# Optimization experiments

Hardware: AMD Instinct MI355X
Metric: run time of the kernel (lower is better)

The kernel has to match this reference:

```python
import jax, jax.numpy as jnp
import numpy as np

B = 16384      # batch size
D = 512        # state_dim (= number of graph nodes)
HID = 512      # hidden_dim of main GCN blocks
EH = 32        # hidden dim of ENSO GCN blocks
K = 2          # fourier_modes
OMEGA = 2.0 * np.pi / 12.0


def setup_inputs() -> dict:
    ks = jax.random.split(jax.random.key(0), 20)
    def w(k, shape, scale=0.05):
        return (jax.random.normal(k, shape) * scale).astype(jnp.float32)
    inp = {
        "x": jax.random.normal(ks[0], (B, D), dtype=jnp.float32),
        "t": jax.random.uniform(ks[1], (1,), dtype=jnp.float32) * 12.0,
        "fourier_coeffs": w(ks[2], (D, D, 2 * K + 1), 0.1),
        # quadratic_graph: GCN(D->HID) -> ReLU -> GCN(HID->D)
        "quad_W1": w(ks[3], (D, HID)), "quad_b1": jnp.zeros((HID,), jnp.float32),
        "quad_W2": w(ks[4], (HID, D)), "quad_b2": jnp.zeros((D,), jnp.float32),
        # cubic_graph
        "cubic_W1": w(ks[5], (D, HID)), "cubic_b1": jnp.zeros((HID,), jnp.float32),
        "cubic_W2": w(ks[6], (HID, D)), "cubic_b2": jnp.zeros((D,), jnp.float32),
        # enso_T_graph: GCN(5->32) -> ReLU -> GCN(32->1)
        "ensoT_W1": w(ks[7], (5, EH)), "ensoT_b1": jnp.zeros((EH,), jnp.float32),
        "ensoT_W2": w(ks[8], (EH, 1)), "ensoT_b2": jnp.zeros((1,), jnp.float32),
        # enso_H_graph
        "ensoH_W1": w(ks[9], (5, EH)), "ensoH_b1": jnp.zeros((EH,), jnp.float32),
        "ensoH_W2": w(ks[10], (EH, 1)), "ensoH_b2": jnp.zeros((1,), jnp.float32),
    }
    return inp


def _gcn2(feat, W1, b1, W2, b2):
    # Fully-connected graph + self-loops => normalized adjacency P = (1/N) 11^T.
    # All node rows are identical (x expanded over nodes), so P @ X == X and every
    # node's output is identical: the 2-layer GCN collapses to two dense GEMMs.
    h = jax.nn.relu(feat @ W1 + b1)
    return h @ W2 + b2


def reference(x, t, fourier_coeffs,
              quad_W1, quad_b1, quad_W2, quad_b2,
              cubic_W1, cubic_b1, cubic_W2, cubic_b2,
              ensoT_W1, ensoT_b1, ensoT_W2, ensoT_b2,
              ensoH_W1, ensoH_b1, ensoH_W2, ensoH_b2):
    ts = t[0]
    # --- Seasonal linear operator L(t) = C0 + sum_k Ck^c cos(k w t) + Ck^s sin(k w t)
    L = fourier_coeffs[:, :, 0]
    for k in range(1, K + 1):
        L = L + fourier_coeffs[:, :, 2 * k - 1] * jnp.cos(k * OMEGA * ts)
        L = L + fourier_coeffs[:, :, 2 * k] * jnp.sin(k * OMEGA * ts)
    linear_term = jnp.einsum('ij,bj->bi', L, x)  # [B, D]

    # --- Graph nonlinear terms (per-node outputs identical; mean over feature dim)
    quad = _gcn2(x, quad_W1, quad_b1, quad_W2, quad_b2)        # [B, D]
    cubic = _gcn2(x, cubic_W1, cubic_b1, cubic_W2, cubic_b2)   # [B, D]
    # torch: out[node] identical for all nodes; .mean(dim=1) over features -> same
    # scalar replicated across the state dimension.
    quad_terms = jnp.broadcast_to(quad.mean(axis=1, keepdims=True), (x.shape[0], D))
    cubic_terms = jnp.broadcast_to(cubic.mean(axis=1, keepdims=True), (x.shape[0], D))
    nonlinear = quad_terms + cubic_terms

    # --- ENSO-specific physics (state_dim >= 2)
    T = x[:, 0:1]
    H = x[:, 1:2]
    fT = jnp.concatenate([T, H, T * T, T * H, T * T * T], axis=1)   # [B, 5]
    fH = jnp.concatenate([T, H, T * T, T * H, T * H * H], axis=1)   # [B, 5]
    cT = _gcn2(fT, ensoT_W1, ensoT_b1, ensoT_W2, ensoT_b2)  # [B, 1]
    cH = _gcn2(fH, ensoH_W1, ensoH_b1, ensoH_W2, ensoH_b2)  # [B, 1]
    pad = jnp.zeros((x.shape[0], D - 2), dtype=x.dtype)
    nonlinear = nonlinear + jnp.concatenate([cT, cH, pad], axis=1)

    return linear_term + nonlinear
```

## Files before the change

### kernel.cpp

```cpp
#include <hip/hip_runtime.h>


#define OMEGA_F 0.5235987755982988f

typedef __attribute__((ext_vector_type(8))) short short8;
typedef __attribute__((ext_vector_type(4))) float f32x4;

__device__ __forceinline__ unsigned short f2bf(float f) {
  union { float f; unsigned int u; } a;
  a.f = f;
  unsigned int u = a.u;
  return (unsigned short)((u + 0x7fffu + ((u >> 16) & 1u)) >> 16);
}

__device__ __forceinline__ void gload16(const void* g, void* l) {
  __builtin_amdgcn_global_load_lds(
      (const __attribute__((address_space(1))) unsigned int*)g,
      (__attribute__((address_space(3))) unsigned int*)l, 16, 0, 0);
}

__global__ void prep_conv(const float* __restrict__ fc, const float* __restrict__ qW1,
                          const float* __restrict__ cW1, const float* __restrict__ t,
                          const float* __restrict__ qW2, const float* __restrict__ cW2,
                          const float* __restrict__ qb2, const float* __restrict__ cb2,
                          const float4* __restrict__ x4, const float* __restrict__ x,
                          const float* __restrict__ tW1, const float* __restrict__ tb1,
                          const float* __restrict__ tW2, const float* __restrict__ tb2,
                          const float* __restrict__ hW1, const float* __restrict__ hb1,
                          const float* __restrict__ hW2, const float* __restrict__ hb2,
                          unsigned short* __restrict__ WT, uint2* __restrict__ xb,
                          float* __restrict__ qw2m, float* __restrict__ cw2m,
                          float* __restrict__ b2m, float* __restrict__ cT,
                          float* __restrict__ cH, float* __restrict__ rowadd) {
  int b = blockIdx.x, tdx = threadIdx.x;
  if (b < 3072) {
    int idx = b * 256 + tdx;
    int n = idx >> 9;
    int k = idx & 511;
    float v;
    if (n < 512) {
      float th = OMEGA_F * t[0];
      float s1, c1, s2, c2;
      sincosf(th, &s1, &c1);
      sincosf(2.0f * th, &s2, &c2);
      const float* p = fc + ((size_t)n * 512 + k) * 5;
      v = p[0] + p[1] * c1 + p[2] * s1 + p[3] * c2 + p[4] * s2;
    } else if (n < 1024) {
      v = qW1[(size_t)k * 512 + (n - 512)];
    } else {
      v = cW1[(size_t)k * 512 + (n - 1024)];
    }
    WT[idx] = f2bf(v);
  } else if (b < 3076) {
    int bb = b - 3072;
    const float* W = (bb < 2) ? qW2 : cW2;
    float* o = (bb < 2) ? qw2m : cw2m;
    int h = (bb & 1) * 256 + tdx;
    const float4* row = (const float4*)(W + (size_t)h * 512);
    float s = 0.f;
    for (int i = 0; i < 128; ++i) { float4 v = row[i]; s += (v.x + v.y) + (v.z + v.w); }
    o[h] = s * (1.0f / 512.0f);
  } else if (b == 3076) {
    __shared__ float sm[256];
    sm[tdx] = qb2[tdx] + qb2[tdx + 256];
    __syncthreads();
    for (int w = 128; w > 0; w >>= 1) { if (tdx < w) sm[tdx] += sm[tdx + w]; __syncthreads(); }
    if (tdx == 0) b2m[0] = sm[0] * (1.0f / 512.0f);
    __syncthreads();
    sm[tdx] = cb2[tdx] + cb2[tdx + 256];
    __syncthreads();
    for (int w = 128; w > 0; w >>= 1) { if (tdx < w) sm[tdx] += sm[tdx + w]; __syncthreads(); }
    if (tdx == 0) b2m[1] = sm[0] * (1.0f / 512.0f);
  } else if (b < 3077 + 8192) {
    int i = (b - 3077) * 256 + tdx;
    float4 v = x4[i];
    uint2 r;
    r.x = (unsigned)f2bf(v.x) | ((unsigned)f2bf(v.y) << 16);
    r.y = (unsigned)f2bf(v.z) | ((unsigned)f2bf(v.w) << 16);
    xb[i] = r;
  } else {
    int row = (b - 11269) * 256 + tdx;
    rowadd[row] = 0.f;
    float T = x[(size_t)row * 512];
    float H = x[(size_t)row * 512 + 1];
    float fT[5] = {T, H, T * T, T * H, T * T * T};
    float fH[5] = {T, H, T * T, T * H, T * H * H};
    float sT = tb2[0], sH = hb2[0];
#pragma unroll 4
    for (int e = 0; e < 32; ++e) {
      float a1 = tb1[e], a2 = hb1[e];
#pragma unroll
      for (int f = 0; f < 5; ++f) {
        a1 += fT[f] * tW1[f * 32 + e];
        a2 += fH[f] * hW1[f * 32 + e];
      }
      sT += fmaxf(a1, 0.f) * tW2[e];
      sH += fmaxf(a2, 0.f) * hW2[e];
    }
    cT[row] = sT;
    cH[row] = sH;
  }
}

#define GEMM_MAINLOOP(A_, Bt_, MB_, NB_)                                          \
  const int tid = threadIdx.x;                                                    \
  const int lane = tid & 63;                                                      \
  const int wave = tid >> 6;                                                      \
  const int wm = wave & 1;                                                        \
  const int wn = wave >> 1;                                                       \
  const int m_base = (MB_);                                                       \
  const int n_base = (NB_);                                                       \
  const int lrow = lane & 15;                                                     \
  const int l7 = lrow & 7;                                                        \
  const int kgrp = lane >> 4;                                                     \
  const int srow = lane >> 3;                                                     \
  const int sk = ((lane & 7) ^ srow) * 8;                                         \
  const unsigned short* gA0 = (A_) + (size_t)(m_base + wave * 8 + srow) * 512 + sk; \
  const unsigned short* gA1 = gA0 + 32 * 512;                                     \
  const unsigned short* gA2 = gA0 + 64 * 512;                                     \
  const unsigned short* gA3 = gA0 + 96 * 512;                                     \
  const unsigned short* gB0 = (Bt_) + (size_t)(n_base + wave * 8 + srow) * 512 + sk;\
  const unsigned short* gB1 = gB0 + 32 * 512;                                     \
  const unsigned short* gB2 = gB0 + 64 * 512;                                     \
  const unsigned short* gB3 = gB0 + 96 * 512;                                     \
  unsigned short* lA0 = As + wave * 512;                                          \
  unsigned short* lA1 = As + (4 + wave) * 512;                                    \
  unsigned short* lA2 = As + (8 + wave) * 512;                                    \
  unsigned short* lA3 = As + (12 + wave) * 512;                                   \
  unsigned short* lB0 = Bs + wave * 512;                                          \
  unsigned short* lB1 = Bs + (4 + wave) * 512;                                    \
  unsigned short* lB2 = Bs + (8 + wave) * 512;                                    \
  unsigned short* lB3 = Bs + (12 + wave) * 512;                                   \
  f32x4 acc[4][4];                                                                \
  _Pragma("unroll") for (int i = 0; i < 4; ++i)                                   \
      _Pragma("unroll") for (int j = 0; j < 4; ++j)                               \
          acc[i][j] = (f32x4){0.f, 0.f, 0.f, 0.f};                                \
  for (int k0 = 0; k0 < 512; k0 += 64) {                                          \
    gload16(gA0, lA0); gload16(gA1, lA1); gload16(gA2, lA2); gload16(gA3, lA3);   \
    gload16(gB0, lB0); gload16(gB1, lB1); gload16(gB2, lB2); gload16(gB3, lB3);   \
    gA0 += 64; gA1 += 64; gA2 += 64; gA3 += 64;                                   \
    gB0 += 64; gB1 += 64; gB2 += 64; gB3 += 64;                                   \
    __syncthreads();                                                              \
    _Pragma("unroll") for (int h = 0; h < 2; ++h) {                               \
      short8 af[4], bfr[4];                                                       \
      const int ks = ((h * 4 + kgrp) ^ l7) * 8;                                   \
      _Pragma("unroll") for (int i = 0; i < 4; ++i)                               \
          af[i] = *(const short8*)(&As[(wm * 64 + i * 16 + lrow) * 64 + ks]);     \
      _Pragma("unroll") for (int j = 0; j < 4; ++j)                               \
          bfr[j] = *(const short8*)(&Bs[(wn * 64 + j * 16 + lrow) * 64 + ks]);    \
      _Pragma("unroll") for (int i = 0; i < 4; ++i)                               \
          _Pragma("unroll") for (int j = 0; j < 4; ++j)                           \
              acc[i][j] = __builtin_amdgcn_mfma_f32_16x16x32_bf16(af[i], bfr[j],  \
                                                                  acc[i][j], 0, 0, 0); \
    }                                                                             \
    __syncthreads();                                                              \
  }

__global__ __launch_bounds__(256) void nl_gemm(
    const unsigned short* __restrict__ A,
    const unsigned short* __restrict__ Bt,
    const float* __restrict__ qb1, const float* __restrict__ cb1,
    const float* __restrict__ qw2m, const float* __restrict__ cw2m,
    float* __restrict__ rowadd) {
  __shared__ unsigned short As[128 * 64];
  __shared__ unsigned short Bs[128 * 64];
  float rs[4][4];
#pragma unroll
  for (int i = 0; i < 4; ++i)
#pragma unroll
    for (int r = 0; r < 4; ++r) rs[i][r] = 0.f;

  for (int t = 0; t < 2; ++t) {
    GEMM_MAINLOOP(A, Bt, blockIdx.x * 128, (blockIdx.y * 2 + t) * 128)
    const bool isq = (n_base < 512);
    const float* b1 = isq ? qb1 : cb1;
    const float* w2m = isq ? qw2m : cw2m;
    const int cb0 = (isq ? n_base : n_base - 512) + wn * 64 + lrow;
#pragma unroll
    for (int j = 0; j < 4; ++j) {
      int col = cb0 + j * 16;
      float bb = b1[col];
      float ww = w2m[col];
#pragma unroll
      for (int i = 0; i < 4; ++i)
#pragma unroll
        for (int r = 0; r < 4; ++r)
          rs[i][r] += fmaxf(acc[i][j][r] + bb, 0.f) * ww;
    }
  }

  const int lane_e = threadIdx.x & 63;
  const int wm_e = (threadIdx.x >> 6) & 1;
  const int rbase = blockIdx.x * 128 + wm_e * 64 + (lane_e >> 4) * 4;
#pragma unroll
  for (int i = 0; i < 4; ++i)
#pragma unroll
    for (int r = 0; r < 4; ++r) {
      float v = rs[i][r];
      v += __shfl_xor(v, 1, 64);
      v += __shfl_xor(v, 2, 64);
      v += __shfl_xor(v, 4, 64);
      v += __shfl_xor(v, 8, 64);
      if ((lane_e & 15) == 0) atomicAdd(&rowadd[rbase + i * 16 + r], v);
    }
}

__global__ __launch_bounds__(256) void lin_gemm(
    const unsigned short* __restrict__ A,
    const unsigned short* __restrict__ Bt,
    const float* __restrict__ rowadd, const float* __restrict__ b2m,
    const float* __restrict__ cT, const float* __restrict__ cH,
    float* __restrict__ out) {
  __shared__ unsigned short As[128 * 64];
  __shared__ unsigned short Bs[128 * 64];
  GEMM_MAINLOOP(A, Bt, blockIdx.x * 128, blockIdx.y * 128)
  const int rbase = m_base + wm * 64 + (lane >> 4) * 4;
  const float b2s = b2m[0] + b2m[1];
  float ra[4][4];
#pragma unroll
  for (int i = 0; i < 4; ++i)
#pragma unroll
    for (int r = 0; r < 4; ++r) ra[i][r] = rowadd[rbase + i * 16 + r] + b2s;
#pragma unroll
  for (int j = 0; j < 4; ++j) {
    int col = n_base + wn * 64 + j * 16 + lrow;
#pragma unroll
    for (int i = 0; i < 4; ++i)
#pragma unroll
      for (int r = 0; r < 4; ++r) {
        int row = rbase + i * 16 + r;
        float v = acc[i][j][r] + ra[i][r];
        if (col == 0) v += cT[row];
        if (col == 1) v += cH[row];
        out[(size_t)row * 512 + col] = v;
      }
  }
}

extern "C" void kernel_launch(void* const* d_in, const int* in_sizes, int n_in,
                              void* d_out, int out_size, void* d_ws, size_t ws_size,
                              hipStream_t stream) {
  const float* x   = (const float*)d_in[0];
  const float* t   = (const float*)d_in[1];
  const float* fc  = (const float*)d_in[2];
  const float* qW1 = (const float*)d_in[3];
  const float* qb1 = (const float*)d_in[4];
  const float* qW2 = (const float*)d_in[5];
  const float* qb2 = (const float*)d_in[6];
  const float* cW1 = (const float*)d_in[7];
  const float* cb1 = (const float*)d_in[8];
  const float* cW2 = (const float*)d_in[9];
  const float* cb2 = (const float*)d_in[10];
  const float* tW1 = (const float*)d_in[11];
  const float* tb1 = (const float*)d_in[12];
  const float* tW2 = (const float*)d_in[13];
  const float* tb2 = (const float*)d_in[14];
  const float* hW1 = (const float*)d_in[15];
  const float* hb1 = (const float*)d_in[16];
  const float* hW2 = (const float*)d_in[17];
  const float* hb2 = (const float*)d_in[18];
  float* out = (float*)d_out;

  char* ws = (char*)d_ws;
  unsigned short* WT = (unsigned short*)(ws);
  unsigned short* xb = (unsigned short*)(ws + 1572864);
  float* qw2m   = (float*)(ws + 18350080);
  float* cw2m   = (float*)(ws + 18352128);
  float* b2m    = (float*)(ws + 18354176);
  float* cT     = (float*)(ws + 18354432);
  float* cH     = (float*)(ws + 18419968);
  float* rowadd = (float*)(ws + 18485504);

  prep_conv<<<11333, 256, 0, stream>>>(fc, qW1, cW1, t, qW2, cW2, qb2, cb2,
                                       (const float4*)x, x,
                                       tW1, tb1, tW2, tb2, hW1, hb1, hW2, hb2,
                                       WT, (uint2*)xb, qw2m, cw2m, b2m, cT, cH,
                                       rowadd);
  nl_gemm<<<dim3(128, 4), 256, 0, stream>>>(xb, WT + (size_t)512 * 512,
                                            qb1, cb1, qw2m, cw2m, rowadd);
  lin_gemm<<<dim3(128, 4), 256, 0, stream>>>(xb, WT, rowadd, b2m, cT, cH, out);
}
```

Before: 171.7 us.

## Fuse nonlinear and linear GEMMs into one kernel with per-row-block counters

Merges the nonlinear GEMM (which reduces into rowadd via atomics) and the linear GEMM into a single kernel. Each block first does its nonlinear share, bumps a per-row-block counter, then runs its linear tile and spin-waits until all four column blocks of that row block have contributed before reading rowadd. This removes one kernel launch and the global barrier between them, and lets the linear GEMM overlap with other blocks' nonlinear work. It relies on all 512 blocks being co-resident (launch_bounds 2 per CU) to avoid deadlock, and adds spin-wait and fence costs.

```diff
diff --git a/kernel.cpp b/kernel.cpp
--- a/kernel.cpp
+++ b/kernel.cpp
@@ -31,7 +31,8 @@
                           unsigned short* __restrict__ WT, uint2* __restrict__ xb,
                           float* __restrict__ qw2m, float* __restrict__ cw2m,
                           float* __restrict__ b2m, float* __restrict__ cT,
-                          float* __restrict__ cH, float* __restrict__ rowadd) {
+                          float* __restrict__ cH, float* __restrict__ rowadd,
+                          unsigned int* __restrict__ cnt) {
   int b = blockIdx.x, tdx = threadIdx.x;
   if (b < 3072) {
     int idx = b * 256 + tdx;
@@ -62,6 +63,7 @@
     o[h] = s * (1.0f / 512.0f);
   } else if (b == 3076) {
     __shared__ float sm[256];
+    if (tdx < 128) cnt[tdx] = 0;
     sm[tdx] = qb2[tdx] + qb2[tdx + 256];
     __syncthreads();
     for (int w = 128; w > 0; w >>= 1) { if (tdx < w) sm[tdx] += sm[tdx + w]; __syncthreads(); }
@@ -156,14 +158,18 @@
     __syncthreads();                                                              \
   }
 
-__global__ __launch_bounds__(256) void nl_gemm(
+__global__ __launch_bounds__(256, 2) void fused_gemm(
     const unsigned short* __restrict__ A,
-    const unsigned short* __restrict__ Bt,
+    const unsigned short* __restrict__ WT,
     const float* __restrict__ qb1, const float* __restrict__ cb1,
     const float* __restrict__ qw2m, const float* __restrict__ cw2m,
-    float* __restrict__ rowadd) {
+    float* __restrict__ rowadd, const float* __restrict__ b2m,
+    const float* __restrict__ cT, const float* __restrict__ cH,
+    float* __restrict__ out, unsigned int* __restrict__ cnt) {
   __shared__ unsigned short As[128 * 64];
   __shared__ unsigned short Bs[128 * 64];
+  const unsigned short* Bnl = WT + (size_t)512 * 512;
+
   float rs[4][4];
 #pragma unroll
   for (int i = 0; i < 4; ++i)
@@ -171,7 +177,7 @@
     for (int r = 0; r < 4; ++r) rs[i][r] = 0.f;
 
   for (int t = 0; t < 2; ++t) {
-    GEMM_MAINLOOP(A, Bt, blockIdx.x * 128, (blockIdx.y * 2 + t) * 128)
+    GEMM_MAINLOOP(A, Bnl, blockIdx.x * 128, (blockIdx.y * 2 + t) * 128)
     const bool isq = (n_base < 512);
     const float* b1 = isq ? qb1 : cb1;
     const float* w2m = isq ? qw2m : cw2m;
@@ -189,51 +195,62 @@
     }
   }
 
-  const int lane_e = threadIdx.x & 63;
-  const int wm_e = (threadIdx.x >> 6) & 1;
-  const int rbase = blockIdx.x * 128 + wm_e * 64 + (lane_e >> 4) * 4;
-#pragma unroll
-  for (int i = 0; i < 4; ++i)
-#pragma unroll
-    for (int r = 0; r < 4; ++r) {
-      float v = rs[i][r];
-      v += __shfl_xor(v, 1, 64);
-      v += __shfl_xor(v, 2, 64);
-      v += __shfl_xor(v, 4, 64);
-      v += __shfl_xor(v, 8, 64);
-      if ((lane_e & 15) == 0) atomicAdd(&rowadd[rbase + i * 16 + r], v);
-    }
-}
-
-__global__ __launch_bounds__(256) void lin_gemm(
-    const unsigned short* __restrict__ A,
-    const unsigned short* __restrict__ Bt,
-    const float* __restrict__ rowadd, const float* __restrict__ b2m,
-    const float* __restrict__ cT, const float* __restrict__ cH,
-    float* __restrict__ out) {
-  __shared__ unsigned short As[128 * 64];
-  __shared__ unsigned short Bs[128 * 64];
-  GEMM_MAINLOOP(A, Bt, blockIdx.x * 128, blockIdx.y * 128)
-  const int rbase = m_base + wm * 64 + (lane >> 4) * 4;
-  const float b2s = b2m[0] + b2m[1];
-  float ra[4][4];
-#pragma unroll
-  for (int i = 0; i < 4; ++i)
-#pragma unroll
-    for (int r = 0; r < 4; ++r) ra[i][r] = rowadd[rbase + i * 16 + r] + b2s;
-#pragma unroll
-  for (int j = 0; j < 4; ++j) {
-    int col = n_base + wn * 64 + j * 16 + lrow;
+  {
+    const int lane_e = threadIdx.x & 63;
+    const int wm_e = (threadIdx.x >> 6) & 1;
+    const int rbase = blockIdx.x * 128 + wm_e * 64 + (lane_e >> 4) * 4;
 #pragma unroll
     for (int i = 0; i < 4; ++i)
 #pragma unroll
       for (int r = 0; r < 4; ++r) {
-        int row = rbase + i * 16 + r;
-        float v = acc[i][j][r] + ra[i][r];
-        if (col == 0) v += cT[row];
-        if (col == 1) v += cH[row];
-        out[(size_t)row * 512 + col] = v;
+        float v = rs[i][r];
+        v += __shfl_xor(v, 1, 64);
+        v += __shfl_xor(v, 2, 64);
+        v += __shfl_xor(v, 4, 64);
+        v += __shfl_xor(v, 8, 64);
+        if ((lane_e & 15) == 0) atomicAdd(&rowadd[rbase + i * 16 + r], v);
       }
+  }
+  __syncthreads();
+  if (threadIdx.x == 0) {
+    __threadfence();
+    atomicAdd(&cnt[blockIdx.x], 1u);
+  }
+
+  {
+    GEMM_MAINLOOP(A, WT, blockIdx.x * 128, blockIdx.y * 128)
+
+    if (wave == 0) {
+      while (__hip_atomic_load(&cnt[blockIdx.x], __ATOMIC_ACQUIRE,
+                               __HIP_MEMORY_SCOPE_AGENT) < 4u) {
+        __builtin_amdgcn_s_sleep(2);
+      }
+    }
+    __syncthreads();
+
+    const int rbase = m_base + wm * 64 + (lane >> 4) * 4;
+    const float b2s = b2m[0] + b2m[1];
+    float ra[4][4];
+#pragma unroll
+    for (int i = 0; i < 4; ++i)
+#pragma unroll
+      for (int r = 0; r < 4; ++r)
+        ra[i][r] = __hip_atomic_load(&rowadd[rbase + i * 16 + r],
+                                     __ATOMIC_RELAXED, __HIP_MEMORY_SCOPE_AGENT) + b2s;
+#pragma unroll
+    for (int j = 0; j < 4; ++j) {
+      int col = n_base + wn * 64 + j * 16 + lrow;
+#pragma unroll
+      for (int i = 0; i < 4; ++i)
+#pragma unroll
+        for (int r = 0; r < 4; ++r) {
+          int row = rbase + i * 16 + r;
+          float v = acc[i][j][r] + ra[i][r];
+          if (col == 0) v += cT[row];
+          if (col == 1) v += cH[row];
+          out[(size_t)row * 512 + col] = v;
+        }
+    }
   }
 }
 
@@ -270,13 +287,13 @@
   float* cT     = (float*)(ws + 18354432);
   float* cH     = (float*)(ws + 18419968);
   float* rowadd = (float*)(ws + 18485504);
+  unsigned int* cnt = (unsigned int*)(ws + 18551040);
 
   prep_conv<<<11333, 256, 0, stream>>>(fc, qW1, cW1, t, qW2, cW2, qb2, cb2,
                                        (const float4*)x, x,
                                        tW1, tb1, tW2, tb2, hW1, hb1, hW2, hb2,
                                        WT, (uint2*)xb, qw2m, cw2m, b2m, cT, cH,
-                                       rowadd);
-  nl_gemm<<<dim3(128, 4), 256, 0, stream>>>(xb, WT + (size_t)512 * 512,
-                                            qb1, cb1, qw2m, cw2m, rowadd);
-  lin_gemm<<<dim3(128, 4), 256, 0, stream>>>(xb, WT, rowadd, b2m, cT, cH, out);
-}
+                                       rowadd, cnt);
+  fused_gemm<<<dim3(128, 4), 256, 0, stream>>>(xb, WT, qb1, cb1, qw2m, cw2m,
+                                               rowadd, b2m, cT, cH, out, cnt);
+}
```

Measured after the change: 182.6 us. 1.06x slower.

## Widen nl_gemm tile to 128x256 so each A tile is loaded once

Applied to the files above, without the earlier changes.

The nonlinear GEMM kernel no longer runs two sequential 128x128 passes over the same A rows. It now loads one A tile and two B tiles per k-step and keeps two sets of accumulators, so each wave does 32 MFMAs per A fragment load. This halves A global/LDS traffic and the number of barrier iterations per block. In exchange it roughly doubles accumulator registers (128 floats per lane) and uses 48KB of LDS, and the launch bound of 2 may cause spills.

```diff
diff --git a/kernel.cpp b/kernel.cpp
--- a/kernel.cpp
+++ b/kernel.cpp
@@ -156,42 +156,120 @@
     __syncthreads();                                                              \
   }
 
-__global__ __launch_bounds__(256) void nl_gemm(
+__global__ __launch_bounds__(256, 2) void nl_gemm(
     const unsigned short* __restrict__ A,
     const unsigned short* __restrict__ Bt,
     const float* __restrict__ qb1, const float* __restrict__ cb1,
     const float* __restrict__ qw2m, const float* __restrict__ cw2m,
     float* __restrict__ rowadd) {
   __shared__ unsigned short As[128 * 64];
-  __shared__ unsigned short Bs[128 * 64];
+  __shared__ unsigned short B0s[128 * 64];
+  __shared__ unsigned short B1s[128 * 64];
+  const int tid = threadIdx.x;
+  const int lane = tid & 63;
+  const int wave = tid >> 6;
+  const int wm = wave & 1;
+  const int wn = wave >> 1;
+  const int m_base = blockIdx.x * 128;
+  const int n0 = blockIdx.y * 256;
+  const int lrow = lane & 15;
+  const int l7 = lrow & 7;
+  const int kgrp = lane >> 4;
+  const int srow = lane >> 3;
+  const int sk = ((lane & 7) ^ srow) * 8;
+
+  const unsigned short* gA0 = A + (size_t)(m_base + wave * 8 + srow) * 512 + sk;
+  const unsigned short* gA1 = gA0 + 32 * 512;
+  const unsigned short* gA2 = gA0 + 64 * 512;
+  const unsigned short* gA3 = gA0 + 96 * 512;
+  const unsigned short* gB00 = Bt + (size_t)(n0 + wave * 8 + srow) * 512 + sk;
+  const unsigned short* gB01 = gB00 + 32 * 512;
+  const unsigned short* gB02 = gB00 + 64 * 512;
+  const unsigned short* gB03 = gB00 + 96 * 512;
+  const unsigned short* gB10 = gB00 + 128 * 512;
+  const unsigned short* gB11 = gB00 + 160 * 512;
+  const unsigned short* gB12 = gB00 + 192 * 512;
+  const unsigned short* gB13 = gB00 + 224 * 512;
+
+  unsigned short* lA0 = As + wave * 512;
+  unsigned short* lA1 = As + (4 + wave) * 512;
+  unsigned short* lA2 = As + (8 + wave) * 512;
+  unsigned short* lA3 = As + (12 + wave) * 512;
+  unsigned short* lB00 = B0s + wave * 512;
+  unsigned short* lB01 = B0s + (4 + wave) * 512;
+  unsigned short* lB02 = B0s + (8 + wave) * 512;
+  unsigned short* lB03 = B0s + (12 + wave) * 512;
+  unsigned short* lB10 = B1s + wave * 512;
+  unsigned short* lB11 = B1s + (4 + wave) * 512;
+  unsigned short* lB12 = B1s + (8 + wave) * 512;
+  unsigned short* lB13 = B1s + (12 + wave) * 512;
+
+  f32x4 acc0[4][4], acc1[4][4];
+#pragma unroll
+  for (int i = 0; i < 4; ++i)
+#pragma unroll
+    for (int j = 0; j < 4; ++j) {
+      acc0[i][j] = (f32x4){0.f, 0.f, 0.f, 0.f};
+      acc1[i][j] = (f32x4){0.f, 0.f, 0.f, 0.f};
+    }
+
+  for (int k0 = 0; k0 < 512; k0 += 64) {
+    gload16(gA0, lA0); gload16(gA1, lA1); gload16(gA2, lA2); gload16(gA3, lA3);
+    gload16(gB00, lB00); gload16(gB01, lB01); gload16(gB02, lB02); gload16(gB03, lB03);
+    gload16(gB10, lB10); gload16(gB11, lB11); gload16(gB12, lB12); gload16(gB13, lB13);
+    gA0 += 64; gA1 += 64; gA2 += 64; gA3 += 64;
+    gB00 += 64; gB01 += 64; gB02 += 64; gB03 += 64;
+    gB10 += 64; gB11 += 64; gB12 += 64; gB13 += 64;
+    __syncthreads();
+#pragma unroll
+    for (int h = 0; h < 2; ++h) {
+      short8 af[4], b0f[4], b1f[4];
+      const int ks = ((h * 4 + kgrp) ^ l7) * 8;
+#pragma unroll
+      for (int i = 0; i < 4; ++i)
+        af[i] = *(const short8*)(&As[(wm * 64 + i * 16 + lrow) * 64 + ks]);
+#pragma unroll
+      for (int j = 0; j < 4; ++j) {
+        b0f[j] = *(const short8*)(&B0s[(wn * 64 + j * 16 + lrow) * 64 + ks]);
+        b1f[j] = *(const short8*)(&B1s[(wn * 64 + j * 16 + lrow) * 64 + ks]);
+      }
+#pragma unroll
+      for (int i = 0; i < 4; ++i)
+#pragma unroll
+        for (int j = 0; j < 4; ++j) {
+          acc0[i][j] = __builtin_amdgcn_mfma_f32_16x16x32_bf16(af[i], b0f[j],
+                                                               acc0[i][j], 0, 0, 0);
+          acc1[i][j] = __builtin_amdgcn_mfma_f32_16x16x32_bf16(af[i], b1f[j],
+                                                               acc1[i][j], 0, 0, 0);
+        }
+    }
+    __syncthreads();
+  }
+
+  const bool isq = (n0 < 512);
+  const float* b1p = isq ? qb1 : cb1;
+  const float* w2m = isq ? qw2m : cw2m;
+  const int cb0 = (isq ? n0 : n0 - 512) + wn * 64 + lrow;
   float rs[4][4];
 #pragma unroll
   for (int i = 0; i < 4; ++i)
 #pragma unroll
     for (int r = 0; r < 4; ++r) rs[i][r] = 0.f;
-
-  for (int t = 0; t < 2; ++t) {
-    GEMM_MAINLOOP(A, Bt, blockIdx.x * 128, (blockIdx.y * 2 + t) * 128)
-    const bool isq = (n_base < 512);
-    const float* b1 = isq ? qb1 : cb1;
-    const float* w2m = isq ? qw2m : cw2m;
-    const int cb0 = (isq ? n_base : n_base - 512) + wn * 64 + lrow;
-#pragma unroll
-    for (int j = 0; j < 4; ++j) {
-      int col = cb0 + j * 16;
-      float bb = b1[col];
-      float ww = w2m[col];
-#pragma unroll
-      for (int i = 0; i < 4; ++i)
-#pragma unroll
-        for (int r = 0; r < 4; ++r)
-          rs[i][r] += fmaxf(acc[i][j][r] + bb, 0.f) * ww;
-    }
-  }
-
-  const int lane_e = threadIdx.x & 63;
-  const int wm_e = (threadIdx.x >> 6) & 1;
-  const int rbase = blockIdx.x * 128 + wm_e * 64 + (lane_e >> 4) * 4;
+#pragma unroll
+  for (int j = 0; j < 4; ++j) {
+    int col0 = cb0 + j * 16;
+    float bb0 = b1p[col0], ww0 = w2m[col0];
+    float bb1 = b1p[col0 + 128], ww1 = w2m[col0 + 128];
+#pragma unroll
+    for (int i = 0; i < 4; ++i)
+#pragma unroll
+      for (int r = 0; r < 4; ++r) {
+        rs[i][r] += fmaxf(acc0[i][j][r] + bb0, 0.f) * ww0;
+        rs[i][r] += fmaxf(acc1[i][j][r] + bb1, 0.f) * ww1;
+      }
+  }
+
+  const int rbase = m_base + wm * 64 + kgrp * 4;
 #pragma unroll
   for (int i = 0; i < 4; ++i)
 #pragma unroll
@@ -201,7 +279,7 @@
       v += __shfl_xor(v, 2, 64);
       v += __shfl_xor(v, 4, 64);
       v += __shfl_xor(v, 8, 64);
-      if ((lane_e & 15) == 0) atomicAdd(&rowadd[rbase + i * 16 + r], v);
+      if (lrow == 0) atomicAdd(&rowadd[rbase + i * 16 + r], v);
     }
 }
 
```

Result: no change. 169.8 us, median of 2 (-1.1%).

## Rewrite nonlinear GEMM as 256x256 tile with 8 waves and 4-stage LDS ring

Applied to the files above, without the earlier changes.

Replaces the 128x128-tile, 4-wave nonlinear GEMM with a 256x256-tile kernel of 8 waves per block. It streams K in 32-wide chunks through a 4-deep swizzled LDS ring using async global-to-LDS loads, fine-grained vmcnt waits and MFMA priority boosting. The goal is more reuse per loaded byte and overlap of memory traffic with MFMA work. In exchange it uses more registers and LDS per block, and the grid shrinks to 256 blocks, which may underfill the CUs.

```diff
diff --git a/kernel.cpp b/kernel.cpp
--- a/kernel.cpp
+++ b/kernel.cpp
@@ -156,44 +156,121 @@
     __syncthreads();                                                              \
   }
 
-__global__ __launch_bounds__(256) void nl_gemm(
+__global__ __launch_bounds__(512, 2) void nl_gemm8(
     const unsigned short* __restrict__ A,
     const unsigned short* __restrict__ Bt,
     const float* __restrict__ qb1, const float* __restrict__ cb1,
     const float* __restrict__ qw2m, const float* __restrict__ cw2m,
     float* __restrict__ rowadd) {
-  __shared__ unsigned short As[128 * 64];
-  __shared__ unsigned short Bs[128 * 64];
-  float rs[4][4];
-#pragma unroll
-  for (int i = 0; i < 4; ++i)
+  __shared__ unsigned short ring[2][4][8192];
+
+  const int tid = threadIdx.x;
+  const int lane = tid & 63;
+  const int wv = tid >> 6;
+  const int wm = wv >> 2;
+  const int wn = wv & 3;
+  const int lrow = lane & 15;
+  const int kgrp = lane >> 4;
+  const int m_base = blockIdx.x * 256;
+  const int n_base = blockIdx.y * 256;
+
+  const int srow0 = wv * 32 + (lane >> 2);
+  const int skc = (lane & 3) ^ ((lane >> 3) & 3);
+  const unsigned short* gA = A + (size_t)(m_base + srow0) * 512 + skc * 8;
+  const unsigned short* gB = Bt + (size_t)(n_base + srow0) * 512 + skc * 8;
+
+#define STAGE_NL(op, s)                                                          \
+  do {                                                                           \
+    unsigned short* _l = &ring[op][(s) & 3][(wv * 32) * 32];                     \
+    const unsigned short* _g = ((op) ? gB : gA) + (s) * 32;                      \
+    gload16(_g, _l);                                                             \
+    gload16(_g + 16 * 512, _l + 16 * 32);                                        \
+  } while (0)
+
+  f32x4 acc[8][4];
+#pragma unroll
+  for (int i = 0; i < 8; ++i)
+#pragma unroll
+    for (int j = 0; j < 4; ++j) acc[i][j] = (f32x4){0.f, 0.f, 0.f, 0.f};
+
+  STAGE_NL(0, 0); STAGE_NL(1, 0);
+  STAGE_NL(0, 1); STAGE_NL(1, 1);
+  STAGE_NL(0, 2); STAGE_NL(1, 2);
+  asm volatile("s_waitcnt vmcnt(4)" ::: "memory");
+  __builtin_amdgcn_s_barrier();
+
+#pragma unroll
+  for (int t = 0; t < 8; ++t) {
+#pragma unroll
+    for (int p = 0; p < 4; ++p) {
+      const int ph = t * 4 + p;
+      const int h = p >> 1;
+      const int ihalf = p & 1;
+      const int ra = (2 * t + h) & 3;
+
+      short8 af[4], bf[4];
+#pragma unroll
+      for (int ii = 0; ii < 4; ++ii) {
+        const int row = wm * 128 + ihalf * 64 + ii * 16 + lrow;
+        const int sw = kgrp ^ ((row >> 1) & 3);
+        af[ii] = *(const short8*)(&ring[0][ra][row * 32 + sw * 8]);
+      }
+#pragma unroll
+      for (int j = 0; j < 4; ++j) {
+        const int row = wn * 64 + j * 16 + lrow;
+        const int sw = kgrp ^ ((row >> 1) & 3);
+        bf[j] = *(const short8*)(&ring[1][ra][row * 32 + sw * 8]);
+      }
+
+      if (ph <= 25) {
+        const int s = (ph >> 1) + 3;
+        if ((ph & 1) == 0) STAGE_NL(0, s);
+        else               STAGE_NL(1, s);
+      }
+
+      if (ph <= 25)      asm volatile("s_waitcnt vmcnt(8)" ::: "memory");
+      else if (ph == 26) asm volatile("s_waitcnt vmcnt(6)" ::: "memory");
+      else if (ph == 27) asm volatile("s_waitcnt vmcnt(4)" ::: "memory");
+      else if (ph == 28) asm volatile("s_waitcnt vmcnt(2)" ::: "memory");
+      else               asm volatile("s_waitcnt vmcnt(0)" ::: "memory");
+      __builtin_amdgcn_s_barrier();
+
+      __builtin_amdgcn_s_setprio(1);
+#pragma unroll
+      for (int ii = 0; ii < 4; ++ii)
+#pragma unroll
+        for (int j = 0; j < 4; ++j)
+          acc[ihalf * 4 + ii][j] = __builtin_amdgcn_mfma_f32_16x16x32_bf16(
+              af[ii], bf[j], acc[ihalf * 4 + ii][j], 0, 0, 0);
+      __builtin_amdgcn_s_setprio(0);
+      __builtin_amdgcn_s_barrier();
+    }
+  }
+#undef STAGE_NL
+
+  const bool isq = (n_base < 512);
+  const float* b1p = isq ? qb1 : cb1;
+  const float* w2m = isq ? qw2m : cw2m;
+  const int cb0 = (isq ? n_base : n_base - 512) + wn * 64 + lrow;
+  float rs[8][4];
+#pragma unroll
+  for (int i = 0; i < 8; ++i)
 #pragma unroll
     for (int r = 0; r < 4; ++r) rs[i][r] = 0.f;
-
-  for (int t = 0; t < 2; ++t) {
-    GEMM_MAINLOOP(A, Bt, blockIdx.x * 128, (blockIdx.y * 2 + t) * 128)
-    const bool isq = (n_base < 512);
-    const float* b1 = isq ? qb1 : cb1;
-    const float* w2m = isq ? qw2m : cw2m;
-    const int cb0 = (isq ? n_base : n_base - 512) + wn * 64 + lrow;
-#pragma unroll
-    for (int j = 0; j < 4; ++j) {
-      int col = cb0 + j * 16;
-      float bb = b1[col];
-      float ww = w2m[col];
-#pragma unroll
-      for (int i = 0; i < 4; ++i)
-#pragma unroll
-        for (int r = 0; r < 4; ++r)
-          rs[i][r] += fmaxf(acc[i][j][r] + bb, 0.f) * ww;
-    }
-  }
-
-  const int lane_e = threadIdx.x & 63;
-  const int wm_e = (threadIdx.x >> 6) & 1;
-  const int rbase = blockIdx.x * 128 + wm_e * 64 + (lane_e >> 4) * 4;
-#pragma unroll
-  for (int i = 0; i < 4; ++i)
+#pragma unroll
+  for (int j = 0; j < 4; ++j) {
+    const int col = cb0 + j * 16;
+    const float bb = b1p[col];
+    const float ww = w2m[col];
+#pragma unroll
+    for (int i = 0; i < 8; ++i)
+#pragma unroll
+      for (int r = 0; r < 4; ++r)
+        rs[i][r] += fmaxf(acc[i][j][r] + bb, 0.f) * ww;
+  }
+  const int rbase = m_base + wm * 128 + kgrp * 4;
+#pragma unroll
+  for (int i = 0; i < 8; ++i)
 #pragma unroll
     for (int r = 0; r < 4; ++r) {
       float v = rs[i][r];
@@ -201,7 +278,7 @@
       v += __shfl_xor(v, 2, 64);
       v += __shfl_xor(v, 4, 64);
       v += __shfl_xor(v, 8, 64);
-      if ((lane_e & 15) == 0) atomicAdd(&rowadd[rbase + i * 16 + r], v);
+      if (lrow == 0) atomicAdd(&rowadd[rbase + i * 16 + r], v);
     }
 }
 
@@ -276,7 +353,7 @@
                                        tW1, tb1, tW2, tb2, hW1, hb1, hW2, hb2,
                                        WT, (uint2*)xb, qw2m, cw2m, b2m, cT, cH,
                                        rowadd);
-  nl_gemm<<<dim3(128, 4), 256, 0, stream>>>(xb, WT + (size_t)512 * 512,
+  nl_gemm8<<<dim3(64, 4), 512, 0, stream>>>(xb, WT + (size_t)512 * 512,
                                             qb1, cb1, qw2m, cw2m, rowadd);
   lin_gemm<<<dim3(128, 4), 256, 0, stream>>>(xb, WT, rowadd, b2m, cT, cH, out);
 }
```

Measured after the change: 169.8 us. About the same (-1.1%).
